# Kernel tuning notes

Hardware: AMD Instinct MI355X
Metric: run time of the kernel (lower is better)

## Reference

```python
import jax, jax.numpy as jnp
import numpy as np

H, D = 12, 768
DH = D // H  # 64

def setup_inputs() -> dict:
    key = jax.random.key(0)
    ks = jax.random.split(key, 9)
    s = 0.02
    x  = jax.random.normal(ks[0], (8, 1024, D), dtype=jnp.float32)
    Wq = jax.random.normal(ks[1], (H, D, DH), dtype=jnp.float32) * s
    Wk = jax.random.normal(ks[2], (H, D, DH), dtype=jnp.float32) * s
    Wv = jax.random.normal(ks[3], (H, D, DH), dtype=jnp.float32) * s
    bq = jax.random.normal(ks[4], (H, DH), dtype=jnp.float32) * s
    bk = jax.random.normal(ks[5], (H, DH), dtype=jnp.float32) * s
    bv = jax.random.normal(ks[6], (H, DH), dtype=jnp.float32) * s
    Wo = jax.random.normal(ks[7], (D, D), dtype=jnp.float32) * s
    bo = jax.random.normal(ks[8], (D,), dtype=jnp.float32) * s
    return {"x": x, "Wq": Wq, "Wk": Wk, "Wv": Wv, "bq": bq, "bk": bk, "bv": bv, "Wo": Wo, "bo": bo}

def reference(x, Wq, Wk, Wv, bq, bk, bv, Wo, bo):
    # x: [B,S,D]; per-head projections batched over heads: [B,H,S,DH]
    q = jnp.einsum('bsd,hde->bhse', x, Wq) + bq[None, :, None, :]
    k = jnp.einsum('bsd,hde->bhse', x, Wk) + bk[None, :, None, :]
    v = jnp.einsum('bsd,hde->bhse', x, Wv) + bv[None, :, None, :]
    scores = jnp.einsum('bhse,bhte->bhst', q, k) / jnp.sqrt(jnp.float32(DH))
    probs = jax.nn.softmax(scores, axis=-1)  # dropout is identity (p=0 / eval)
    ctx = jnp.einsum('bhst,bhte->bhse', probs, v)  # [B,H,S,DH]
    B, _, S, _ = ctx.shape
    # concat heads along feature dim (head order matches torch cat order)
    ctx = jnp.transpose(ctx, (0, 2, 1, 3)).reshape(B, S, H * DH)
    out = jnp.einsum('bsd,de->bse', ctx, Wo) + bo
    return out
```

## Files before the change

### kernel.cpp

```cpp
#include <hip/hip_runtime.h>
#include <math.h>


constexpr int NB  = 8;
constexpr int SEQ = 1024;
constexpr int NH  = 12;
constexpr int DM  = 768;
constexpr int DHD = 64;
constexpr int MROWS = NB * SEQ;
constexpr int NQKV  = 3 * NH * DHD;

typedef __attribute__((ext_vector_type(8))) short short8;
typedef __attribute__((ext_vector_type(4))) float f32x4;

#define MFMA16(a,b,c) __builtin_amdgcn_mfma_f32_16x16x32_bf16((a),(b),(c),0,0,0)

#if __has_builtin(__builtin_amdgcn_exp2f)
#define EXP2(x) __builtin_amdgcn_exp2f(x)
#else
#define EXP2(x) exp2f(x)
#endif

__device__ __forceinline__ unsigned short f2bf(float f) {
    unsigned u = __float_as_uint(f);
    return (unsigned short)((u + 0x7fffu + ((u >> 16) & 1u)) >> 16);
}
__device__ __forceinline__ unsigned short f2bf_fast(float f) {
    return (unsigned short)((__float_as_uint(f) + 0x8000u) >> 16);
}

__device__ __forceinline__ void gl_lds16(const unsigned short* g, unsigned short* l) {
    __builtin_amdgcn_global_load_lds(
        (const __attribute__((address_space(1))) void*)g,
        (__attribute__((address_space(3))) void*)l, 16, 0, 0);
}

__device__ __forceinline__ void stageK(unsigned short* lds, const unsigned short* gbase,
                                       int i, int ln, int ldg) {
    int r    = i * 8 + (ln >> 3);
    int cpos = ln & 7;
    int cdat = (cpos - r) & 7;
    gl_lds16(gbase + (size_t)r * ldg + cdat * 8, lds + i * 512);
}
__device__ __forceinline__ short8 ldK(const unsigned short* buf, int row, int chunk) {
    int c = (chunk + row) & 7;
    return *(const short8*)&buf[row * 64 + c * 8];
}

__global__ __launch_bounds__(256) void prep_k(
    const float* __restrict__ x,
    const float* __restrict__ Wq, const float* __restrict__ Wk,
    const float* __restrict__ Wv, const float* __restrict__ Wo,
    unsigned short* __restrict__ xb, unsigned short* __restrict__ wt,
    unsigned short* __restrict__ wot) {
    __shared__ float tb[64][65];
    const int blk = blockIdx.x, tid = threadIdx.x;
    if (blk < 6144) {
        const int i = blk * 256 + tid;
        float4 v = ((const float4*)x)[i];
        ushort4 o;
        o.x = f2bf(v.x); o.y = f2bf(v.y); o.z = f2bf(v.z); o.w = f2bf(v.w);
        ((ushort4*)xb)[i] = o;
        return;
    }
    const int t = blk - 6144;
    const int job = t / 144, lb = t % 144;
    const float* W;
    unsigned short* dst;
    int C, r0, c0;
    if (job < 3) {
        const float* Ws = (job == 0) ? Wq : (job == 1 ? Wk : Wv);
        const int h = lb / 12, rb = lb % 12;
        W = Ws + (size_t)h * (DM * DHD);
        dst = wt + (size_t)(job * 12 + h) * (DM * DHD);
        C = DHD; r0 = rb * 64; c0 = 0;
    } else {
        W = Wo; dst = wot; C = DM;
        r0 = (lb / 12) * 64; c0 = (lb % 12) * 64;
    }
    const int rr = tid >> 2, cc = (tid & 3) * 16;
#pragma unroll
    for (int j = 0; j < 16; j += 4) {
        float4 v = *(const float4*)&W[(size_t)(r0 + rr) * C + c0 + cc + j];
        tb[rr][cc + j + 0] = v.x;
        tb[rr][cc + j + 1] = v.y;
        tb[rr][cc + j + 2] = v.z;
        tb[rr][cc + j + 3] = v.w;
    }
    __syncthreads();
#pragma unroll
    for (int j = 0; j < 16; ++j)
        dst[(size_t)(c0 + rr) * DM + r0 + cc + j] = f2bf(tb[cc + j][rr]);
}

__global__ __launch_bounds__(256, 3) void qkv_mfma_k(
    const unsigned short* __restrict__ xb, const unsigned short* __restrict__ wt,
    const float* __restrict__ bq, const float* __restrict__ bk, const float* __restrict__ bv,
    unsigned short* __restrict__ qb, unsigned short* __restrict__ kb,
    unsigned short* __restrict__ vT) {
    __shared__ unsigned short Ah[128 * 64], Bh[128 * 64];

    const int tid = threadIdx.x;
    const int wv = tid >> 6, ln = tid & 63, quad = ln >> 4, lnid = ln & 15;
    const int wvm = wv >> 1, wvn = wv & 1;
    const int row0 = blockIdx.x * 128, col0 = blockIdx.y * 128;
    const int sel = (col0 >= 2 * DM) ? 2 : (col0 >= DM ? 1 : 0);

    f32x4 acc[4][4];
#pragma unroll
    for (int i = 0; i < 4; ++i)
#pragma unroll
        for (int j = 0; j < 4; ++j) acc[i][j] = (f32x4){0.f, 0.f, 0.f, 0.f};

    const unsigned short* Ahg = xb + (size_t)row0 * DM;
    const unsigned short* Bhg = wt + (size_t)col0 * DM;
    constexpr int NIT = DM / 64;

    if (sel < 2) {
        for (int it = 0; it < NIT; ++it) {
            const int kc = it * 64;
            __syncthreads();
#pragma unroll
            for (int c = 0; c < 4; ++c) {
                stageK(Ah, Ahg + kc, wv * 4 + c, ln, DM);
                stageK(Bh, Bhg + kc, wv * 4 + c, ln, DM);
            }
            __syncthreads();
#pragma unroll
            for (int ks = 0; ks < 2; ++ks) {
                short8 a[4], b[4];
#pragma unroll
                for (int i = 0; i < 4; ++i)
                    a[i] = ldK(Ah, wvm * 64 + i * 16 + lnid, ks * 4 + quad);
#pragma unroll
                for (int j = 0; j < 4; ++j)
                    b[j] = ldK(Bh, wvn * 64 + j * 16 + lnid, ks * 4 + quad);
#pragma unroll
                for (int j = 0; j < 4; ++j)
#pragma unroll
                    for (int i = 0; i < 4; ++i)
                        acc[j][i] = MFMA16(b[j], a[i], acc[j][i]);
            }
        }
        const float scale = (sel == 0) ? 0.18033688011112042f : 1.0f;
        const float* bias = (sel == 0) ? bq : bk;
        unsigned short* oh = (sel == 0) ? qb : kb;
#pragma unroll
        for (int et = 0; et < 4; ++et) {
            const int e = col0 + wvn * 64 + et * 16 + quad * 4;
            const int he = e - sel * DM;
            const int hh2 = he >> 6, ee = he & 63;
            float4 bs = *(const float4*)&bias[he];
#pragma unroll
            for (int st = 0; st < 4; ++st) {
                const int srow = row0 + wvm * 64 + st * 16 + lnid;
                const int bb = srow >> 10, ss = srow & (SEQ - 1);
                ushort4 pk;
                pk.x = f2bf((acc[et][st][0] + bs.x) * scale);
                pk.y = f2bf((acc[et][st][1] + bs.y) * scale);
                pk.z = f2bf((acc[et][st][2] + bs.z) * scale);
                pk.w = f2bf((acc[et][st][3] + bs.w) * scale);
                *(ushort4*)&oh[((size_t)(bb * NH + hh2) * SEQ + ss) * DHD + ee] = pk;
            }
        }
    } else {
        for (int it = 0; it < NIT; ++it) {
            const int kc = it * 64;
            __syncthreads();
#pragma unroll
            for (int c = 0; c < 4; ++c) {
                stageK(Ah, Ahg + kc, wv * 4 + c, ln, DM);
                stageK(Bh, Bhg + kc, wv * 4 + c, ln, DM);
            }
            __syncthreads();
#pragma unroll
            for (int ks = 0; ks < 2; ++ks) {
                short8 a[4], b[4];
#pragma unroll
                for (int i = 0; i < 4; ++i)
                    a[i] = ldK(Ah, wvm * 64 + i * 16 + lnid, ks * 4 + quad);
#pragma unroll
                for (int j = 0; j < 4; ++j)
                    b[j] = ldK(Bh, wvn * 64 + j * 16 + lnid, ks * 4 + quad);
#pragma unroll
                for (int i = 0; i < 4; ++i)
#pragma unroll
                    for (int j = 0; j < 4; ++j)
                        acc[i][j] = MFMA16(a[i], b[j], acc[i][j]);
            }
        }
#pragma unroll
        for (int i = 0; i < 4; ++i) {
#pragma unroll
            for (int j = 0; j < 4; ++j) {
                const int col = col0 + wvn * 64 + j * 16 + lnid;
                const int he = col - 2 * DM;
                const int hh2 = he >> 6, ee = he & 63;
                const float bs = bv[he];
                const int srow = row0 + wvm * 64 + i * 16 + quad * 4;
                const int bb = srow >> 10, ss = srow & (SEQ - 1);
                ushort4 pk;
                pk.x = f2bf(acc[i][j][0] + bs);
                pk.y = f2bf(acc[i][j][1] + bs);
                pk.z = f2bf(acc[i][j][2] + bs);
                pk.w = f2bf(acc[i][j][3] + bs);
                *(ushort4*)&vT[((size_t)(bb * NH + hh2) * DHD + ee) * SEQ + ss] = pk;
            }
        }
    }
}

__global__ __launch_bounds__(512, 6) void attn_mfma_k(
    const unsigned short* __restrict__ qb, const unsigned short* __restrict__ kb,
    const unsigned short* __restrict__ vT, unsigned short* __restrict__ ctb) {
    __shared__ unsigned short ksh[2][64 * 64], vsm[2][64 * 64];
    __shared__ unsigned short ps[128 * 64];

    const int tid = threadIdx.x;
    const int wv = tid >> 6, ln = tid & 63, quad = ln >> 4, lnid = ln & 15;
    const int bhid = blockIdx.x % 96, qt = blockIdx.x / 96;
    const int b = bhid / NH, h = bhid % NH;
    const int q0 = qt * 128;
    const unsigned short* qhb = qb + (size_t)bhid * (SEQ * DHD);
    const unsigned short* khb = kb + (size_t)bhid * (SEQ * DHD);
    const unsigned short* vTb = vT + (size_t)bhid * (DHD * SEQ);

    const int prow = wv * 16 + lnid;

    short8 qf[2];
#pragma unroll
    for (int ks_ = 0; ks_ < 2; ++ks_)
        qf[ks_] = *(const short8*)(qhb + (size_t)(q0 + prow) * DHD + ks_ * 32 + quad * 8);

    f32x4 ctx[4];
#pragma unroll
    for (int j = 0; j < 4; ++j) ctx[j] = (f32x4){0.f, 0.f, 0.f, 0.f};
    float lsum = 0.f;

    stageK(ksh[0], khb, wv, ln, DHD);
    stageK(vsm[0], vTb, wv, ln, SEQ);

    for (int kt = 0; kt < SEQ / 64; ++kt) {
        const int cur = kt & 1;
        __syncthreads();
        if (kt + 1 < SEQ / 64) {
            stageK(ksh[cur ^ 1], khb + (kt + 1) * 64 * DHD, wv, ln, DHD);
            stageK(vsm[cur ^ 1], vTb + (kt + 1) * 64, wv, ln, SEQ);
        }

        f32x4 sc[4];
#pragma unroll
        for (int j = 0; j < 4; ++j) sc[j] = (f32x4){0.f, 0.f, 0.f, 0.f};
#pragma unroll
        for (int ks_ = 0; ks_ < 2; ++ks_) {
#pragma unroll
            for (int nt = 0; nt < 4; ++nt) {
                short8 kf = ldK(ksh[cur], nt * 16 + lnid, ks_ * 4 + quad);
                sc[nt] = MFMA16(kf, qf[ks_], sc[nt]);
            }
        }

#pragma unroll
        for (int nt = 0; nt < 4; ++nt) {
            float p0 = EXP2(sc[nt][0]);
            float p1 = EXP2(sc[nt][1]);
            float p2 = EXP2(sc[nt][2]);
            float p3 = EXP2(sc[nt][3]);
            lsum += (p0 + p1) + (p2 + p3);
            ushort4 pw;
            pw.x = f2bf_fast(p0);
            pw.y = f2bf_fast(p1);
            pw.z = f2bf_fast(p2);
            pw.w = f2bf_fast(p3);
            const int cpos = (2 * nt + (quad >> 1) + prow) & 7;
            *(ushort4*)&ps[prow * 64 + cpos * 8 + (quad & 1) * 4] = pw;
        }

#pragma unroll
        for (int kvs = 0; kvs < 2; ++kvs) {
            short8 pf = ldK(ps, prow, kvs * 4 + quad);
#pragma unroll
            for (int dt = 0; dt < 4; ++dt) {
                short8 vf = ldK(vsm[cur], dt * 16 + lnid, kvs * 4 + quad);
                ctx[dt] = MFMA16(vf, pf, ctx[dt]);
            }
        }
    }

    float s = lsum;
    s += __shfl_xor(s, 16, 64);
    s += __shfl_xor(s, 32, 64);
    const float inv = 1.0f / s;
    const int srow = b * SEQ + q0 + prow;
#pragma unroll
    for (int dt = 0; dt < 4; ++dt) {
        ushort4 pk;
        pk.x = f2bf(ctx[dt][0] * inv);
        pk.y = f2bf(ctx[dt][1] * inv);
        pk.z = f2bf(ctx[dt][2] * inv);
        pk.w = f2bf(ctx[dt][3] * inv);
        *(ushort4*)&ctb[(size_t)srow * DM + h * DHD + dt * 16 + quad * 4] = pk;
    }
}

__global__ __launch_bounds__(256, 3) void out_mfma_k(
    const unsigned short* __restrict__ ctb, const unsigned short* __restrict__ wot,
    const float* __restrict__ bo, float* __restrict__ out) {
    __shared__ unsigned short Ah[128 * 64], Bh[64 * 64];

    const int tid = threadIdx.x;
    const int wv = tid >> 6, ln = tid & 63, quad = ln >> 4, lnid = ln & 15;
    const int wvm = wv >> 1, wvn = wv & 1;
    const int row0 = blockIdx.x * 128, col0 = blockIdx.y * 64;

    f32x4 acc[2][4];
#pragma unroll
    for (int j = 0; j < 2; ++j)
#pragma unroll
        for (int i = 0; i < 4; ++i) acc[j][i] = (f32x4){0.f, 0.f, 0.f, 0.f};

    const unsigned short* Ahg = ctb + (size_t)row0 * DM;
    const unsigned short* Bhg = wot + (size_t)col0 * DM;

    constexpr int NIT = DM / 64;
    for (int it = 0; it < NIT; ++it) {
        const int kc = it * 64;
        __syncthreads();
#pragma unroll
        for (int c = 0; c < 4; ++c) stageK(Ah, Ahg + kc, wv * 4 + c, ln, DM);
#pragma unroll
        for (int c = 0; c < 2; ++c) stageK(Bh, Bhg + kc, wv * 2 + c, ln, DM);
        __syncthreads();
#pragma unroll
        for (int ks = 0; ks < 2; ++ks) {
            short8 a[4], b[2];
#pragma unroll
            for (int i = 0; i < 4; ++i)
                a[i] = ldK(Ah, wvm * 64 + i * 16 + lnid, ks * 4 + quad);
#pragma unroll
            for (int j = 0; j < 2; ++j)
                b[j] = ldK(Bh, wvn * 32 + j * 16 + lnid, ks * 4 + quad);
#pragma unroll
            for (int j = 0; j < 2; ++j)
#pragma unroll
                for (int i = 0; i < 4; ++i)
                    acc[j][i] = MFMA16(b[j], a[i], acc[j][i]);
        }
    }

#pragma unroll
    for (int jt = 0; jt < 2; ++jt) {
        const int colb = col0 + wvn * 32 + jt * 16 + quad * 4;
        float4 bs = *(const float4*)&bo[colb];
#pragma unroll
        for (int it = 0; it < 4; ++it) {
            const int srow = row0 + wvm * 64 + it * 16 + lnid;
            float4 o;
            o.x = acc[jt][it][0] + bs.x;
            o.y = acc[jt][it][1] + bs.y;
            o.z = acc[jt][it][2] + bs.z;
            o.w = acc[jt][it][3] + bs.w;
            *(float4*)&out[(size_t)srow * DM + colb] = o;
        }
    }
}

extern "C" void kernel_launch(void* const* d_in, const int* in_sizes, int n_in,
                              void* d_out, int out_size, void* d_ws, size_t ws_size,
                              hipStream_t stream) {
    const float* x  = (const float*)d_in[0];
    const float* Wq = (const float*)d_in[1];
    const float* Wk = (const float*)d_in[2];
    const float* Wv = (const float*)d_in[3];
    const float* bq = (const float*)d_in[4];
    const float* bk = (const float*)d_in[5];
    const float* bv = (const float*)d_in[6];
    const float* Wo = (const float*)d_in[7];
    const float* bo = (const float*)d_in[8];
    float* out = (float*)d_out;

    char* w = (char*)d_ws;
    const size_t elsX = (size_t)MROWS * DM;
    const size_t elsQ = (size_t)NB * NH * SEQ * DHD;
    unsigned short* xb  = (unsigned short*)w;
    unsigned short* ctb = xb;
    size_t off = elsX * 2;
    unsigned short* wt  = (unsigned short*)(w + off); off += (size_t)NQKV * DM * 2;
    unsigned short* wot = (unsigned short*)(w + off); off += (size_t)DM * DM * 2;
    unsigned short* qbp = (unsigned short*)(w + off); off += elsQ * 2;
    unsigned short* kbp = (unsigned short*)(w + off); off += elsQ * 2;
    unsigned short* vTp = (unsigned short*)(w + off); off += elsQ * 2;

    prep_k<<<dim3(6144 + 576), 256, 0, stream>>>(x, Wq, Wk, Wv, Wo, xb, wt, wot);
    qkv_mfma_k<<<dim3(MROWS / 128, NQKV / 128), 256, 0, stream>>>(
        xb, wt, bq, bk, bv, qbp, kbp, vTp);
    attn_mfma_k<<<dim3(768), 512, 0, stream>>>(qbp, kbp, vTp, ctb);
    out_mfma_k<<<dim3(MROWS / 128, DM / 64), 256, 0, stream>>>(ctb, wot, bo, out);
}
```

Before: 193.9 us.

## Use 32x32 MFMA in attention and enlarge QKV GEMM tile to 256 rows

The attention kernel moves from 16x16x32 to 32x32x16 bf16 MFMA, with each of 4 waves owning 32 query rows instead of 8 waves owning 16. K/V staging, the P tile layout and the output indexing are remapped to match, which cuts LDS fragment reads per flop. The QKV projection kernel grows to 512 threads and 256-row tiles so weight tiles are reused across more rows. The larger tiles raise register and LDS pressure and halve the QKV grid, which may lower occupancy.

```diff
diff --git a/kernel.cpp b/kernel.cpp
--- a/kernel.cpp
+++ b/kernel.cpp
@@ -12,8 +12,10 @@
 
 typedef __attribute__((ext_vector_type(8))) short short8;
 typedef __attribute__((ext_vector_type(4))) float f32x4;
+typedef __attribute__((ext_vector_type(16))) float f32x16;
 
 #define MFMA16(a,b,c) __builtin_amdgcn_mfma_f32_16x16x32_bf16((a),(b),(c),0,0,0)
+#define MFMA32(a,b,c) __builtin_amdgcn_mfma_f32_32x32x16_bf16((a),(b),(c),0,0,0)
 
 #if __has_builtin(__builtin_amdgcn_exp2f)
 #define EXP2(x) __builtin_amdgcn_exp2f(x)
@@ -93,17 +95,17 @@
         dst[(size_t)(c0 + rr) * DM + r0 + cc + j] = f2bf(tb[cc + j][rr]);
 }
 
-__global__ __launch_bounds__(256, 3) void qkv_mfma_k(
+__global__ __launch_bounds__(512, 4) void qkv_mfma_k(
     const unsigned short* __restrict__ xb, const unsigned short* __restrict__ wt,
     const float* __restrict__ bq, const float* __restrict__ bk, const float* __restrict__ bv,
     unsigned short* __restrict__ qb, unsigned short* __restrict__ kb,
     unsigned short* __restrict__ vT) {
-    __shared__ unsigned short Ah[128 * 64], Bh[128 * 64];
+    __shared__ unsigned short Ah[256 * 64], Bh[128 * 64];
 
     const int tid = threadIdx.x;
     const int wv = tid >> 6, ln = tid & 63, quad = ln >> 4, lnid = ln & 15;
     const int wvm = wv >> 1, wvn = wv & 1;
-    const int row0 = blockIdx.x * 128, col0 = blockIdx.y * 128;
+    const int row0 = blockIdx.x * 256, col0 = blockIdx.y * 128;
     const int sel = (col0 >= 2 * DM) ? 2 : (col0 >= DM ? 1 : 0);
 
     f32x4 acc[4][4];
@@ -121,10 +123,9 @@
             const int kc = it * 64;
             __syncthreads();
 #pragma unroll
-            for (int c = 0; c < 4; ++c) {
-                stageK(Ah, Ahg + kc, wv * 4 + c, ln, DM);
-                stageK(Bh, Bhg + kc, wv * 4 + c, ln, DM);
-            }
+            for (int c = 0; c < 4; ++c) stageK(Ah, Ahg + kc, wv * 4 + c, ln, DM);
+#pragma unroll
+            for (int c = 0; c < 2; ++c) stageK(Bh, Bhg + kc, wv * 2 + c, ln, DM);
             __syncthreads();
 #pragma unroll
             for (int ks = 0; ks < 2; ++ks) {
@@ -168,10 +169,9 @@
             const int kc = it * 64;
             __syncthreads();
 #pragma unroll
-            for (int c = 0; c < 4; ++c) {
-                stageK(Ah, Ahg + kc, wv * 4 + c, ln, DM);
-                stageK(Bh, Bhg + kc, wv * 4 + c, ln, DM);
-            }
+            for (int c = 0; c < 4; ++c) stageK(Ah, Ahg + kc, wv * 4 + c, ln, DM);
+#pragma unroll
+            for (int c = 0; c < 2; ++c) stageK(Bh, Bhg + kc, wv * 2 + c, ln, DM);
             __syncthreads();
 #pragma unroll
             for (int ks = 0; ks < 2; ++ks) {
@@ -210,14 +210,15 @@
     }
 }
 
-__global__ __launch_bounds__(512, 6) void attn_mfma_k(
+__global__ __launch_bounds__(256, 3) void attn_mfma_k(
     const unsigned short* __restrict__ qb, const unsigned short* __restrict__ kb,
     const unsigned short* __restrict__ vT, unsigned short* __restrict__ ctb) {
     __shared__ unsigned short ksh[2][64 * 64], vsm[2][64 * 64];
     __shared__ unsigned short ps[128 * 64];
 
     const int tid = threadIdx.x;
-    const int wv = tid >> 6, ln = tid & 63, quad = ln >> 4, lnid = ln & 15;
+    const int wv = tid >> 6, ln = tid & 63;
+    const int l32 = ln & 31, lh = ln >> 5;
     const int bhid = blockIdx.x % 96, qt = blockIdx.x / 96;
     const int b = bhid / NH, h = bhid % NH;
     const int q0 = qt * 128;
@@ -225,81 +226,93 @@
     const unsigned short* khb = kb + (size_t)bhid * (SEQ * DHD);
     const unsigned short* vTb = vT + (size_t)bhid * (DHD * SEQ);
 
-    const int prow = wv * 16 + lnid;
-
-    short8 qf[2];
-#pragma unroll
-    for (int ks_ = 0; ks_ < 2; ++ks_)
-        qf[ks_] = *(const short8*)(qhb + (size_t)(q0 + prow) * DHD + ks_ * 32 + quad * 8);
-
-    f32x4 ctx[4];
-#pragma unroll
-    for (int j = 0; j < 4; ++j) ctx[j] = (f32x4){0.f, 0.f, 0.f, 0.f};
+    const int qrow = wv * 32 + l32;
+
+    short8 qf[4];
+#pragma unroll
+    for (int kci = 0; kci < 4; ++kci)
+        qf[kci] = *(const short8*)(qhb + (size_t)(q0 + qrow) * DHD + kci * 16 + lh * 8);
+
+    f32x16 ctx[2];
+    ctx[0] = (f32x16)(0.0f);
+    ctx[1] = (f32x16)(0.0f);
     float lsum = 0.f;
 
-    stageK(ksh[0], khb, wv, ln, DHD);
-    stageK(vsm[0], vTb, wv, ln, SEQ);
+    stageK(ksh[0], khb, wv * 2, ln, DHD);
+    stageK(ksh[0], khb, wv * 2 + 1, ln, DHD);
+    stageK(vsm[0], vTb, wv * 2, ln, SEQ);
+    stageK(vsm[0], vTb, wv * 2 + 1, ln, SEQ);
 
     for (int kt = 0; kt < SEQ / 64; ++kt) {
         const int cur = kt & 1;
         __syncthreads();
         if (kt + 1 < SEQ / 64) {
-            stageK(ksh[cur ^ 1], khb + (kt + 1) * 64 * DHD, wv, ln, DHD);
-            stageK(vsm[cur ^ 1], vTb + (kt + 1) * 64, wv, ln, SEQ);
-        }
-
-        f32x4 sc[4];
-#pragma unroll
-        for (int j = 0; j < 4; ++j) sc[j] = (f32x4){0.f, 0.f, 0.f, 0.f};
-#pragma unroll
-        for (int ks_ = 0; ks_ < 2; ++ks_) {
-#pragma unroll
-            for (int nt = 0; nt < 4; ++nt) {
-                short8 kf = ldK(ksh[cur], nt * 16 + lnid, ks_ * 4 + quad);
-                sc[nt] = MFMA16(kf, qf[ks_], sc[nt]);
-            }
-        }
-
-#pragma unroll
-        for (int nt = 0; nt < 4; ++nt) {
-            float p0 = EXP2(sc[nt][0]);
-            float p1 = EXP2(sc[nt][1]);
-            float p2 = EXP2(sc[nt][2]);
-            float p3 = EXP2(sc[nt][3]);
-            lsum += (p0 + p1) + (p2 + p3);
-            ushort4 pw;
-            pw.x = f2bf_fast(p0);
-            pw.y = f2bf_fast(p1);
-            pw.z = f2bf_fast(p2);
-            pw.w = f2bf_fast(p3);
-            const int cpos = (2 * nt + (quad >> 1) + prow) & 7;
-            *(ushort4*)&ps[prow * 64 + cpos * 8 + (quad & 1) * 4] = pw;
-        }
-
-#pragma unroll
-        for (int kvs = 0; kvs < 2; ++kvs) {
-            short8 pf = ldK(ps, prow, kvs * 4 + quad);
-#pragma unroll
-            for (int dt = 0; dt < 4; ++dt) {
-                short8 vf = ldK(vsm[cur], dt * 16 + lnid, kvs * 4 + quad);
-                ctx[dt] = MFMA16(vf, pf, ctx[dt]);
-            }
-        }
-    }
-
-    float s = lsum;
-    s += __shfl_xor(s, 16, 64);
-    s += __shfl_xor(s, 32, 64);
+            const unsigned short* kn = khb + (kt + 1) * 64 * DHD;
+            const unsigned short* vn = vTb + (kt + 1) * 64;
+            stageK(ksh[cur ^ 1], kn, wv * 2, ln, DHD);
+            stageK(ksh[cur ^ 1], kn, wv * 2 + 1, ln, DHD);
+            stageK(vsm[cur ^ 1], vn, wv * 2, ln, SEQ);
+            stageK(vsm[cur ^ 1], vn, wv * 2 + 1, ln, SEQ);
+        }
+
+        f32x16 sc[2];
+        sc[0] = (f32x16)(0.0f);
+        sc[1] = (f32x16)(0.0f);
+#pragma unroll
+        for (int kci = 0; kci < 4; ++kci) {
+#pragma unroll
+            for (int jt = 0; jt < 2; ++jt) {
+                short8 kf = ldK(ksh[cur], jt * 32 + l32, 2 * kci + lh);
+                sc[jt] = MFMA32(kf, qf[kci], sc[jt]);
+            }
+        }
+
+#pragma unroll
+        for (int jt = 0; jt < 2; ++jt) {
+#pragma unroll
+            for (int rg = 0; rg < 4; ++rg) {
+                float p0 = EXP2(sc[jt][rg * 4 + 0]);
+                float p1 = EXP2(sc[jt][rg * 4 + 1]);
+                float p2 = EXP2(sc[jt][rg * 4 + 2]);
+                float p3 = EXP2(sc[jt][rg * 4 + 3]);
+                lsum += (p0 + p1) + (p2 + p3);
+                ushort4 pw;
+                pw.x = f2bf_fast(p0);
+                pw.y = f2bf_fast(p1);
+                pw.z = f2bf_fast(p2);
+                pw.w = f2bf_fast(p3);
+                const int cdat = jt * 4 + rg;
+                const int cpos = (cdat + qrow) & 7;
+                *(ushort4*)&ps[qrow * 64 + cpos * 8 + lh * 4] = pw;
+            }
+        }
+
+#pragma unroll
+        for (int jk = 0; jk < 4; ++jk) {
+            short8 pf = ldK(ps, qrow, 2 * jk + lh);
+#pragma unroll
+            for (int dt = 0; dt < 2; ++dt) {
+                short8 vf = ldK(vsm[cur], dt * 32 + l32, 2 * jk + lh);
+                ctx[dt] = MFMA32(vf, pf, ctx[dt]);
+            }
+        }
+    }
+
+    float s = lsum + __shfl_xor(lsum, 32, 64);
     const float inv = 1.0f / s;
-    const int srow = b * SEQ + q0 + prow;
-#pragma unroll
-    for (int dt = 0; dt < 4; ++dt) {
-        ushort4 pk;
-        pk.x = f2bf(ctx[dt][0] * inv);
-        pk.y = f2bf(ctx[dt][1] * inv);
-        pk.z = f2bf(ctx[dt][2] * inv);
-        pk.w = f2bf(ctx[dt][3] * inv);
-        *(ushort4*)&ctb[(size_t)srow * DM + h * DHD + dt * 16 + quad * 4] = pk;
+    const int srow = b * SEQ + q0 + qrow;
+#pragma unroll
+    for (int dt = 0; dt < 2; ++dt) {
+#pragma unroll
+        for (int rg = 0; rg < 4; ++rg) {
+            ushort4 pk;
+            pk.x = f2bf(ctx[dt][rg * 4 + 0] * inv);
+            pk.y = f2bf(ctx[dt][rg * 4 + 1] * inv);
+            pk.z = f2bf(ctx[dt][rg * 4 + 2] * inv);
+            pk.w = f2bf(ctx[dt][rg * 4 + 3] * inv);
+            const int d = dt * 32 + 8 * rg + 4 * lh;
+            *(ushort4*)&ctb[(size_t)srow * DM + h * DHD + d] = pk;
+        }
     }
 }
 
@@ -392,8 +405,8 @@
     unsigned short* vTp = (unsigned short*)(w + off); off += elsQ * 2;
 
     prep_k<<<dim3(6144 + 576), 256, 0, stream>>>(x, Wq, Wk, Wv, Wo, xb, wt, wot);
-    qkv_mfma_k<<<dim3(MROWS / 128, NQKV / 128), 256, 0, stream>>>(
+    qkv_mfma_k<<<dim3(MROWS / 256, NQKV / 128), 512, 0, stream>>>(
         xb, wt, bq, bk, bv, qbp, kbp, vTp);
-    attn_mfma_k<<<dim3(768), 512, 0, stream>>>(qbp, kbp, vTp, ctb);
+    attn_mfma_k<<<dim3(768), 256, 0, stream>>>(qbp, kbp, vTp, ctb);
     out_mfma_k<<<dim3(MROWS / 128, DM / 64), 256, 0, stream>>>(ctb, wot, bo, out);
 }
```

After: 228.2 us. 17.7% more time.
